# Kernel optimization log

Measured on AMD Instinct MI355X. Metric: run time of the kernel, lower is better.

## Reference

```python
import jax, jax.numpy as jnp
import numpy as np

B, S, D, H, DFF = 2, 2048, 768, 12, 3072
DK = D // H
EPS = 1e-6


def setup_inputs() -> dict:
    key = jax.random.key(0)
    ks = jax.random.split(key, 12)
    n = lambda k, shp: jax.random.normal(k, shp, jnp.float32) * 0.02
    return {
        "x": jax.random.normal(ks[0], (B, S, D), jnp.float32),
        "mask": jax.random.randint(ks[1], (1, 1, S, S), 0, 2).astype(jnp.int32),
        "wq": n(ks[2], (D, D)), "bq": jnp.zeros((D,), jnp.float32),
        "wk": n(ks[3], (D, D)), "bk": jnp.zeros((D,), jnp.float32),
        "wv": n(ks[4], (D, D)), "bv": jnp.zeros((D,), jnp.float32),
        "wo": n(ks[5], (D, D)), "bo": jnp.zeros((D,), jnp.float32),
        "w1": n(ks[6], (D, DFF)), "b1": jnp.zeros((DFF,), jnp.float32),
        "w2": n(ks[7], (DFF, D)), "b2": jnp.zeros((D,), jnp.float32),
        "alpha1": jnp.ones((D,), jnp.float32), "beta1": jnp.zeros((D,), jnp.float32),
        "alpha2": jnp.ones((D,), jnp.float32), "beta2": jnp.zeros((D,), jnp.float32),
    }


def _layernorm(x, alpha, bias):
    # Faithful to source: unbiased std (ddof=1) and eps added to std, not var.
    mean = x.mean(axis=-1, keepdims=True)
    var = jnp.sum((x - mean) ** 2, axis=-1, keepdims=True) / (x.shape[-1] - 1)
    return alpha * (x - mean) / (jnp.sqrt(var) + EPS) + bias


def reference(x, mask, wq, bq, wk, bk, wv, bv, wo, bo, w1, b1, w2, b2,
              alpha1, beta1, alpha2, beta2):
    # --- residual 1: pre-norm self-attention ---
    h = _layernorm(x, alpha1, beta1)
    q = (h @ wq + bq).reshape(B, S, H, DK).transpose(0, 2, 1, 3)  # [B,H,S,DK]
    k = (h @ wk + bk).reshape(B, S, H, DK).transpose(0, 2, 1, 3)
    v = (h @ wv + bv).reshape(B, S, H, DK).transpose(0, 2, 1, 3)
    scores = jnp.einsum('bhsd,bhtd->bhst', q, k) / jnp.sqrt(jnp.float32(DK))
    scores = jnp.where(mask == 0, jnp.float32(-1e9), scores)
    attn = jax.nn.softmax(scores, axis=-1)
    o = jnp.einsum('bhst,bhtd->bhsd', attn, v)
    o = o.transpose(0, 2, 1, 3).reshape(B, S, D)
    x = x + (o @ wo + bo)
    # --- residual 2: pre-norm FFN ---
    h2 = _layernorm(x, alpha2, beta2)
    ff = jnp.maximum(h2 @ w1 + b1, 0.0) @ w2 + b2
    return x + ff
```

## Files before the change

### kernel.cpp

```cpp
#include <hip/hip_runtime.h>

typedef unsigned short u16;
typedef unsigned int u32;
typedef unsigned long long u64;
typedef __attribute__((ext_vector_type(8))) short bf16x8;
typedef __attribute__((ext_vector_type(4))) float f32x4;
typedef __attribute__((ext_vector_type(2))) unsigned int u32x2;

#define SEQ 2048
#define DM  768
#define NH  12
#define NB  2
#define LDQ (3 * DM)

#define SCALE_Q 0.180336879f
#define NEGB   -1.44269504e9f

__device__ __forceinline__ float bf2f(u16 u) {
  union { u32 i; float f; } v; v.i = ((u32)u) << 16; return v.f;
}
__device__ __forceinline__ u16 f2bf(float f) {
  union { float f; u32 i; } v; v.f = f;
  u32 r = v.i + 0x7FFFu + ((v.i >> 16) & 1u);
  return (u16)(r >> 16);
}
__device__ __forceinline__ void gl_lds16(const u16* g, u16* l) {
  __builtin_amdgcn_global_load_lds(
      (const __attribute__((address_space(1))) unsigned int*)g,
      (__attribute__((address_space(3))) unsigned int*)l, 16, 0, 0);
}

__global__ __launch_bounds__(256) void prep_kernel(
    const float* __restrict__ wq, const float* __restrict__ wk,
    const float* __restrict__ wv, const float* __restrict__ wo,
    const float* __restrict__ w1, const float* __restrict__ w2,
    const float* __restrict__ bq, const float* __restrict__ bk,
    const float* __restrict__ bv, const int* __restrict__ mask,
    u16* __restrict__ wqkvt, u16* __restrict__ wot,
    u16* __restrict__ w1t, u16* __restrict__ w2t,
    float* __restrict__ bqkv, u64* __restrict__ mbitsT) {
  __shared__ float t[32][33];
  const int j = blockIdx.x, tid = threadIdx.x;
  const float* in = nullptr; u16* out = nullptr;
  int R = 0, C = 0, bx = 0, by = 0; float sc = 1.0f;
  if (j < 2304) {
    int which = j / 576, local = j % 576;
    in = which == 0 ? wq : which == 1 ? wk : which == 2 ? wv : wo;
    out = which == 3 ? wot : wqkvt + (size_t)which * DM * DM;
    sc = (which == 0) ? SCALE_Q : 1.0f;
    R = DM; C = DM; bx = local % 24; by = local / 24;
  } else if (j < 4608) {
    int local = j - 2304;
    in = w1; out = w1t; R = DM; C = 3072; bx = local % 96; by = local / 96;
  } else if (j < 6912) {
    int local = j - 4608;
    in = w2; out = w2t; R = 3072; C = DM; bx = local % 24; by = local / 24;
  } else if (j < 6921) {
    int i = (j - 6912) * 256 + tid;
    float v = (i < DM) ? bq[i] * SCALE_Q : (i < 2 * DM ? bk[i - DM] : bv[i - 2 * DM]);
    bqkv[i] = v;
    return;
  } else {
    int wid = (j - 6921) * 4 + (tid >> 6);
    int lane = tid & 63;
    int row = wid >> 5, word = wid & 31;
    int m = mask[(long)row * SEQ + word * 64 + lane];
    u64 bb = __ballot(m != 0);
    if (lane == 0) mbitsT[(long)word * SEQ + row] = bb;
    return;
  }
  long r0 = (long)by * 32, c0 = (long)bx * 32;
  int lc = tid & 31, wr = tid >> 5;
#pragma unroll
  for (int i = 0; i < 4; i++) {
    int row = wr + i * 8;
    t[row][lc] = in[(r0 + row) * C + c0 + lc];
  }
  __syncthreads();
#pragma unroll
  for (int i = 0; i < 4; i++) {
    int row = wr + i * 8;
    out[(c0 + row) * R + r0 + lc] = f2bf(t[lc][row] * sc);
  }
}

__global__ __launch_bounds__(256) void transpose_kernel(
    const u16* __restrict__ in, u16* __restrict__ out, int ldin, int R, int C) {
  __shared__ u16 t[32][33];
  long r0 = (long)blockIdx.y * 32, c0 = (long)blockIdx.x * 32;
  int lc = threadIdx.x & 31, wr = threadIdx.x >> 5;
#pragma unroll
  for (int i = 0; i < 4; i++) {
    int row = wr + i * 8;
    t[row][lc] = in[(r0 + row) * (long)ldin + c0 + lc];
  }
  __syncthreads();
#pragma unroll
  for (int i = 0; i < 4; i++) {
    int row = wr + i * 8;
    out[(c0 + row) * R + r0 + lc] = t[lc][row];
  }
}

__global__ __launch_bounds__(256) void ln_kernel(
    const float* __restrict__ x, const float* __restrict__ alpha,
    const float* __restrict__ beta, u16* __restrict__ out) {
  long row = blockIdx.x;
  const float* xr = x + row * DM;
  int tid = threadIdx.x;
  float v[3];
  float s = 0.f, sq = 0.f;
#pragma unroll
  for (int i = 0; i < 3; i++) {
    v[i] = xr[tid + i * 256];
    s += v[i]; sq += v[i] * v[i];
  }
#pragma unroll
  for (int off = 32; off >= 1; off >>= 1) {
    s += __shfl_down(s, off, 64);
    sq += __shfl_down(sq, off, 64);
  }
  __shared__ float ss[4], ssq[4];
  int wave = tid >> 6;
  if ((tid & 63) == 0) { ss[wave] = s; ssq[wave] = sq; }
  __syncthreads();
  float ts = ss[0] + ss[1] + ss[2] + ss[3];
  float tsq = ssq[0] + ssq[1] + ssq[2] + ssq[3];
  float mean = ts * (1.0f / (float)DM);
  float var = fmaxf((tsq - ts * mean) * (1.0f / (float)(DM - 1)), 0.0f);
  float inv = 1.0f / (sqrtf(var) + 1e-6f);
#pragma unroll
  for (int i = 0; i < 3; i++) {
    int c = tid + i * 256;
    out[row * DM + c] = f2bf(alpha[c] * (v[i] - mean) * inv + beta[c]);
  }
}

template<int BN>
__global__ __launch_bounds__(256, 2) void gemm_bt_kernel(
    const u16* __restrict__ A, const u16* __restrict__ Bt,
    const float* __restrict__ bias, const float* res,
    u16* Cb, float* Cf, int M, int N, int K, int relu) {
  constexpr int NJ = BN / 32;
  __shared__ __align__(16) u16 As[2][128][32];
  __shared__ __align__(16) u16 Bs[2][BN][32];
  const int tid = threadIdx.x;
  const int lane = tid & 63, wave = tid >> 6;
  const int g = lane >> 4, lr = lane & 15;
  const int wm = (wave >> 1) * 64, wn = (wave & 1) * (BN / 2);
  const long m0 = (long)blockIdx.y * 128;
  const long n0 = (long)blockIdx.x * BN;
  const int srow = tid >> 2;
  const int scol = (tid & 3) * 8;

  const u16* aSrc = A + (m0 + srow) * K + scol;
  const u16* bSrc = Bt + (n0 + srow) * K + scol;

  auto STAGE = [&](int buf, int k0) {
    gl_lds16(aSrc + k0, &As[buf][srow][scol]);
    gl_lds16(aSrc + (long)64 * K + k0, &As[buf][srow + 64][scol]);
    gl_lds16(bSrc + k0, &Bs[buf][srow][scol]);
    if (BN == 128) gl_lds16(bSrc + (long)64 * K + k0, &Bs[buf][srow + 64][scol]);
  };

  f32x4 acc[4][NJ];
#pragma unroll
  for (int i = 0; i < 4; i++)
#pragma unroll
    for (int j = 0; j < NJ; j++) acc[i][j] = (f32x4)0.0f;

  STAGE(0, 0);
  __syncthreads();
  const int nk = K / 32;
  for (int t = 0; t < nk; t++) {
    const int cur = t & 1;
    if (t + 1 < nk) STAGE(cur ^ 1, (t + 1) * 32);
    bf16x8 af[4], bfr[NJ];
#pragma unroll
    for (int i = 0; i < 4; i++) af[i] = *(const bf16x8*)&As[cur][wm + i * 16 + lr][g * 8];
#pragma unroll
    for (int j = 0; j < NJ; j++) bfr[j] = *(const bf16x8*)&Bs[cur][wn + j * 16 + lr][g * 8];
#pragma unroll
    for (int i = 0; i < 4; i++)
#pragma unroll
      for (int j = 0; j < NJ; j++)
        acc[i][j] = __builtin_amdgcn_mfma_f32_16x16x32_bf16(af[i], bfr[j], acc[i][j], 0, 0, 0);
    __syncthreads();
  }
#pragma unroll
  for (int j = 0; j < NJ; j++) {
    long col = n0 + wn + j * 16 + lr;
    float bv = bias[col];
#pragma unroll
    for (int i = 0; i < 4; i++) {
#pragma unroll
      for (int r = 0; r < 4; r++) {
        long row = m0 + wm + i * 16 + g * 4 + r;
        float v = acc[i][j][r] + bv;
        if (res) v += res[row * N + col];
        if (relu) v = fmaxf(v, 0.0f);
        if (Cb) Cb[row * N + col] = f2bf(v);
        else    Cf[row * N + col] = v;
      }
    }
  }
}

__global__ __launch_bounds__(256, 3) void attn_kernel(
    const u16* __restrict__ qkv, const u16* __restrict__ vt,
    const u64* __restrict__ mbitsT, u16* __restrict__ o) {
  __shared__ __align__(16) u16 Ks[2][64][64];
  __shared__ __align__(16) u16 Vs[2][64][64];
  __shared__ __align__(16) u32 Ps32[4][16][32];
  const int qt = blockIdx.x, h = blockIdx.y, b = blockIdx.z;
  const int tid = threadIdx.x;
  const int lane = tid & 63, wave = tid >> 6;
  const int g = lane >> 4, lr = lane & 15;
  const int qr0 = qt * 64 + wave * 16;

  const u16* q = qkv;
  const u16* k = qkv + DM;

  const long qbase = ((long)(b * SEQ + qr0 + lr)) * LDQ + h * 64;
  bf16x8 qf0 = *(const bf16x8*)(q + qbase + g * 8);
  bf16x8 qf1 = *(const bf16x8*)(q + qbase + 32 + g * 8);

  bf16x8 onesf;
#pragma unroll
  for (int j = 0; j < 8; j++) onesf[j] = (short)0x3F80;

  f32x4 lsum = (f32x4)0.0f;
  f32x4 oacc[4];
#pragma unroll
  for (int d = 0; d < 4; d++) oacc[d] = (f32x4)0.0f;

  const int strow = tid >> 3;
  const int stcolb = (tid & 7) * 16;
  const int swzb = stcolb ^ ((strow & 7) << 4);
  const u16* ksrc = k + (long)b * SEQ * LDQ + h * 64 + (swzb >> 1);
  const u16* vsrc = vt + ((long)(h * 64 + strow)) * (NB * SEQ) + (long)b * SEQ + (swzb >> 1);
  const int sc16 = stcolb >> 1;

  auto STAGE = [&](int buf, int kt) {
    const u16* kr = ksrc + (long)(kt * 64 + strow) * LDQ;
    gl_lds16(kr, &Ks[buf][strow][sc16]);
    gl_lds16(kr + (long)32 * LDQ, &Ks[buf][strow + 32][sc16]);
    const u16* vr = vsrc + kt * 64;
    gl_lds16(vr, &Vs[buf][strow][sc16]);
    gl_lds16(vr + 32 * (NB * SEQ), &Vs[buf][strow + 32][sc16]);
  };

  const int rs = (lr & 7) << 3;
  const int c0 = (g * 8) ^ rs;
  const int c1 = (32 + g * 8) ^ rs;

  const u64* mrow = mbitsT + (qr0 + lr);
  const int pswz = (lr & 7) << 2;
  const int pb0 = (4 * g) ^ pswz;
  const int pb1 = (16 + 4 * g) ^ pswz;

  STAGE(0, 0);
  __syncthreads();
  for (int kt = 0; kt < SEQ / 64; kt++) {
    const int cur = kt & 1;
    if (kt + 1 < SEQ / 64) STAGE(cur ^ 1, kt + 1);
    u64 mb = mrow[(long)kt * SEQ];

    f32x4 sf[4];
    __builtin_amdgcn_s_setprio(1);
#pragma unroll
    for (int n = 0; n < 4; n++) {
      bf16x8 kb0 = *(const bf16x8*)&Ks[cur][n * 16 + lr][c0];
      bf16x8 kb1 = *(const bf16x8*)&Ks[cur][n * 16 + lr][c1];
      sf[n] = __builtin_amdgcn_mfma_f32_16x16x32_bf16(kb0, qf0, (f32x4)0.0f, 0, 0, 0);
      sf[n] = __builtin_amdgcn_mfma_f32_16x16x32_bf16(kb1, qf1, sf[n], 0, 0, 0);
    }
    __builtin_amdgcn_s_setprio(0);
    u64 tsh = mb >> (4 * g);
    u32 mlo = (u32)tsh, mhi = (u32)(tsh >> 32);
#pragma unroll
    for (int n = 0; n < 4; n++) {
      u32 w = (n < 2) ? mlo : mhi;
#pragma unroll
      for (int r = 0; r < 4; r++) {
        u32 bit = 1u << (16 * (n & 1) + r);
        sf[n][r] = (w & bit) ? sf[n][r] : NEGB;
      }
    }
#pragma unroll
    for (int n = 0; n < 4; n++) {
      union { float f; u32 i; } p0, p1, p2, p3;
      p0.f = exp2f(sf[n][0]); p1.f = exp2f(sf[n][1]);
      p2.f = exp2f(sf[n][2]); p3.f = exp2f(sf[n][3]);
      u32 w0 = (p1.i & 0xFFFF0000u) | (p0.i >> 16);
      u32 w1 = (p3.i & 0xFFFF0000u) | (p2.i >> 16);
      int widx = (8 * n + 2 * g) ^ pswz;
      *(u32x2*)&Ps32[wave][lr][widx] = (u32x2){w0, w1};
    }
    asm volatile("" ::: "memory");
    bf16x8 pf0 = *(const bf16x8*)&Ps32[wave][lr][pb0];
    bf16x8 pf1 = *(const bf16x8*)&Ps32[wave][lr][pb1];
    __builtin_amdgcn_s_setprio(1);
    lsum = __builtin_amdgcn_mfma_f32_16x16x32_bf16(onesf, pf0, lsum, 0, 0, 0);
    lsum = __builtin_amdgcn_mfma_f32_16x16x32_bf16(onesf, pf1, lsum, 0, 0, 0);
#pragma unroll
    for (int db = 0; db < 4; db++) {
      bf16x8 v0 = *(const bf16x8*)&Vs[cur][db * 16 + lr][c0];
      bf16x8 v1 = *(const bf16x8*)&Vs[cur][db * 16 + lr][c1];
      oacc[db] = __builtin_amdgcn_mfma_f32_16x16x32_bf16(v0, pf0, oacc[db], 0, 0, 0);
      oacc[db] = __builtin_amdgcn_mfma_f32_16x16x32_bf16(v1, pf1, oacc[db], 0, 0, 0);
    }
    __builtin_amdgcn_s_setprio(0);
    __syncthreads();
  }
  float inv = 1.0f / lsum[0];
  long row = (long)b * SEQ + qr0 + lr;
#pragma unroll
  for (int db = 0; db < 4; db++) {
    u32 lo = ((u32)f2bf(oacc[db][1] * inv) << 16) | f2bf(oacc[db][0] * inv);
    u32 hi = ((u32)f2bf(oacc[db][3] * inv) << 16) | f2bf(oacc[db][2] * inv);
    *(u32x2*)(o + row * DM + h * 64 + db * 16 + g * 4) = (u32x2){lo, hi};
  }
}

extern "C" void kernel_launch(void* const* d_in, const int* in_sizes, int n_in,
                              void* d_out, int out_size, void* d_ws, size_t ws_size,
                              hipStream_t stream) {
  const float* x      = (const float*)d_in[0];
  const int*   mask   = (const int*)d_in[1];
  const float* wq     = (const float*)d_in[2];
  const float* bq     = (const float*)d_in[3];
  const float* wk     = (const float*)d_in[4];
  const float* bk     = (const float*)d_in[5];
  const float* wv     = (const float*)d_in[6];
  const float* bv     = (const float*)d_in[7];
  const float* wo     = (const float*)d_in[8];
  const float* bo     = (const float*)d_in[9];
  const float* w1     = (const float*)d_in[10];
  const float* b1     = (const float*)d_in[11];
  const float* w2     = (const float*)d_in[12];
  const float* b2     = (const float*)d_in[13];
  const float* alpha1 = (const float*)d_in[14];
  const float* beta1  = (const float*)d_in[15];
  const float* alpha2 = (const float*)d_in[16];
  const float* beta2  = (const float*)d_in[17];
  float* outf = (float*)d_out;

  char* ws = (char*)d_ws;
  size_t off = 0;
  auto alloc = [&](size_t bytes) {
    void* p = ws + off;
    off += (bytes + 255) & ~(size_t)255;
    return p;
  };
  const size_t DD = (size_t)DM * DM * 2;
  const size_t DF = (size_t)DM * 3072 * 2;
  const size_t ROWS = (size_t)NB * SEQ;
  const size_t ACT = ROWS * DM * 2;

  u16* wqkvt = (u16*)alloc(3 * DD);
  u16* wot   = (u16*)alloc(DD);
  u16* w1t   = (u16*)alloc(DF);
  u16* w2t   = (u16*)alloc(DF);
  float* bqkv = (float*)alloc(3 * DM * 4);
  u64* mbitsT = (u64*)alloc((size_t)(SEQ / 64) * SEQ * 8);
  u16* h     = (u16*)alloc(ACT);
  u16* qkv   = (u16*)alloc(ROWS * 3 * DM * 2);
  u16* vtb   = (u16*)alloc(ACT);
  u16* ob    = (u16*)alloc(ACT);
  u16* fb = qkv;
  u16* h2 = h;
  float* x1 = outf;

  dim3 blk(256);
  prep_kernel<<<dim3(23305), blk, 0, stream>>>(wq, wk, wv, wo, w1, w2, bq, bk, bv,
                                               mask, wqkvt, wot, w1t, w2t, bqkv, mbitsT);

  ln_kernel<<<ROWS, blk, 0, stream>>>(x, alpha1, beta1, h);
  gemm_bt_kernel<128><<<dim3(18, 32), blk, 0, stream>>>(h, wqkvt, bqkv, nullptr, qkv, nullptr, 4096, 3 * DM, 768, 0);
  transpose_kernel<<<dim3(24, 128), blk, 0, stream>>>(qkv + 2 * DM, vtb, LDQ, 4096, 768);
  attn_kernel<<<dim3(SEQ / 64, NH, NB), blk, 0, stream>>>(qkv, vtb, mbitsT, ob);
  gemm_bt_kernel<64><<<dim3(12, 32), blk, 0, stream>>>(ob, wot, bo, x, nullptr, x1, 4096, 768, 768, 0);
  ln_kernel<<<ROWS, blk, 0, stream>>>(x1, alpha2, beta2, h2);
  gemm_bt_kernel<128><<<dim3(24, 32), blk, 0, stream>>>(h2, w1t, b1, nullptr, fb, nullptr, 4096, 3072, 768, 1);
  gemm_bt_kernel<64><<<dim3(12, 32), blk, 0, stream>>>(fb, w2t, b2, x1, nullptr, outf, 4096, 768, 3072, 0);
}
```

Before: 238.3 us.

## Triple-buffer GEMM loads with vmcnt waits and remap blocks across XCDs

The GEMM kernel moves from double to triple buffering in LDS. It waits on outstanding vector-memory counts with explicit s_waitcnt and uses one barrier per k-step instead of two syncthreads, so loads for tile t+2 overlap compute on tile t. GEMM and attention launches become 1D grids with a block-index swizzle that places neighbouring tiles on the same XCD, aiming for better L2 reuse. The cost is more LDS per block and hand-tuned wait counts, which must match the number of loads each STAGE issues.

Result: faster. 220.7 us (-7.4%).

```diff
diff --git a/kernel.cpp b/kernel.cpp
--- a/kernel.cpp
+++ b/kernel.cpp
@@ -28,6 +28,11 @@
   __builtin_amdgcn_global_load_lds(
       (const __attribute__((address_space(1))) unsigned int*)g,
       (__attribute__((address_space(3))) unsigned int*)l, 16, 0, 0);
+}
+template<int N> __device__ __forceinline__ void wait_vmcnt() {
+  if constexpr (N == 0) asm volatile("s_waitcnt vmcnt(0)" ::: "memory");
+  else if constexpr (N == 3) asm volatile("s_waitcnt vmcnt(3)" ::: "memory");
+  else if constexpr (N == 4) asm volatile("s_waitcnt vmcnt(4)" ::: "memory");
 }
 
 __global__ __launch_bounds__(256) void prep_kernel(
@@ -140,23 +145,28 @@
 __global__ __launch_bounds__(256, 2) void gemm_bt_kernel(
     const u16* __restrict__ A, const u16* __restrict__ Bt,
     const float* __restrict__ bias, const float* res,
-    u16* Cb, float* Cf, int M, int N, int K, int relu) {
+    u16* Cb, float* Cf, int M, int N, int K, int relu, int nx) {
   constexpr int NJ = BN / 32;
-  __shared__ __align__(16) u16 As[2][128][32];
-  __shared__ __align__(16) u16 Bs[2][BN][32];
+  constexpr int L = (BN == 128) ? 4 : 3;
+  __shared__ __align__(16) u16 As[3][128][32];
+  __shared__ __align__(16) u16 Bs[3][BN][32];
   const int tid = threadIdx.x;
   const int lane = tid & 63, wave = tid >> 6;
   const int g = lane >> 4, lr = lane & 15;
   const int wm = (wave >> 1) * 64, wn = (wave & 1) * (BN / 2);
-  const long m0 = (long)blockIdx.y * 128;
-  const long n0 = (long)blockIdx.x * BN;
+  const int o = blockIdx.x;
+  const int wg = (o & 7) * ((int)gridDim.x >> 3) + (o >> 3);
+  const int bx = wg % nx, by = wg / nx;
+  const long m0 = (long)by * 128;
+  const long n0 = (long)bx * BN;
   const int srow = tid >> 2;
   const int scol = (tid & 3) * 8;
 
   const u16* aSrc = A + (m0 + srow) * K + scol;
   const u16* bSrc = Bt + (n0 + srow) * K + scol;
 
-  auto STAGE = [&](int buf, int k0) {
+  auto STAGE = [&](int buf, int t) {
+    const int k0 = t * 32;
     gl_lds16(aSrc + k0, &As[buf][srow][scol]);
     gl_lds16(aSrc + (long)64 * K + k0, &As[buf][srow + 64][scol]);
     gl_lds16(bSrc + k0, &Bs[buf][srow][scol]);
@@ -169,12 +179,14 @@
 #pragma unroll
     for (int j = 0; j < NJ; j++) acc[i][j] = (f32x4)0.0f;
 
+  const int nk = K / 32;
   STAGE(0, 0);
-  __syncthreads();
-  const int nk = K / 32;
+  STAGE(1, 1);
   for (int t = 0; t < nk; t++) {
-    const int cur = t & 1;
-    if (t + 1 < nk) STAGE(cur ^ 1, (t + 1) * 32);
+    const int cur = t % 3;
+    if (t + 1 < nk) wait_vmcnt<L>(); else wait_vmcnt<0>();
+    __builtin_amdgcn_sched_barrier(0);
+    __builtin_amdgcn_s_barrier();
     bf16x8 af[4], bfr[NJ];
 #pragma unroll
     for (int i = 0; i < 4; i++) af[i] = *(const bf16x8*)&As[cur][wm + i * 16 + lr][g * 8];
@@ -185,7 +197,7 @@
 #pragma unroll
       for (int j = 0; j < NJ; j++)
         acc[i][j] = __builtin_amdgcn_mfma_f32_16x16x32_bf16(af[i], bfr[j], acc[i][j], 0, 0, 0);
-    __syncthreads();
+    if (t + 2 < nk) STAGE((t + 2) % 3, t + 2);
   }
 #pragma unroll
   for (int j = 0; j < NJ; j++) {
@@ -208,11 +220,13 @@
 
 __global__ __launch_bounds__(256, 3) void attn_kernel(
     const u16* __restrict__ qkv, const u16* __restrict__ vt,
-    const u64* __restrict__ mbitsT, u16* __restrict__ o) {
+    const u64* __restrict__ mbitsT, u16* __restrict__ o_) {
   __shared__ __align__(16) u16 Ks[2][64][64];
   __shared__ __align__(16) u16 Vs[2][64][64];
   __shared__ __align__(16) u32 Ps32[4][16][32];
-  const int qt = blockIdx.x, h = blockIdx.y, b = blockIdx.z;
+  const int o = blockIdx.x;
+  const int wg = (o & 7) * 96 + (o >> 3);
+  const int qt = wg & 31, h = (wg >> 5) % NH, b = wg / (32 * NH);
   const int tid = threadIdx.x;
   const int lane = tid & 63, wave = tid >> 6;
   const int g = lane >> 4, lr = lane & 15;
@@ -319,7 +333,7 @@
   for (int db = 0; db < 4; db++) {
     u32 lo = ((u32)f2bf(oacc[db][1] * inv) << 16) | f2bf(oacc[db][0] * inv);
     u32 hi = ((u32)f2bf(oacc[db][3] * inv) << 16) | f2bf(oacc[db][2] * inv);
-    *(u32x2*)(o + row * DM + h * 64 + db * 16 + g * 4) = (u32x2){lo, hi};
+    *(u32x2*)(o_ + row * DM + h * 64 + db * 16 + g * 4) = (u32x2){lo, hi};
   }
 }
 
@@ -377,11 +391,11 @@
                                                mask, wqkvt, wot, w1t, w2t, bqkv, mbitsT);
 
   ln_kernel<<<ROWS, blk, 0, stream>>>(x, alpha1, beta1, h);
-  gemm_bt_kernel<128><<<dim3(18, 32), blk, 0, stream>>>(h, wqkvt, bqkv, nullptr, qkv, nullptr, 4096, 3 * DM, 768, 0);
+  gemm_bt_kernel<128><<<dim3(576), blk, 0, stream>>>(h, wqkvt, bqkv, nullptr, qkv, nullptr, 4096, 3 * DM, 768, 0, 18);
   transpose_kernel<<<dim3(24, 128), blk, 0, stream>>>(qkv + 2 * DM, vtb, LDQ, 4096, 768);
-  attn_kernel<<<dim3(SEQ / 64, NH, NB), blk, 0, stream>>>(qkv, vtb, mbitsT, ob);
-  gemm_bt_kernel<64><<<dim3(12, 32), blk, 0, stream>>>(ob, wot, bo, x, nullptr, x1, 4096, 768, 768, 0);
+  attn_kernel<<<dim3(32 * NH * NB), blk, 0, stream>>>(qkv, vtb, mbitsT, ob);
+  gemm_bt_kernel<64><<<dim3(384), blk, 0, stream>>>(ob, wot, bo, x, nullptr, x1, 4096, 768, 768, 0, 12);
   ln_kernel<<<ROWS, blk, 0, stream>>>(x1, alpha2, beta2, h2);
-  gemm_bt_kernel<128><<<dim3(24, 32), blk, 0, stream>>>(h2, w1t, b1, nullptr, fb, nullptr, 4096, 3072, 768, 1);
-  gemm_bt_kernel<64><<<dim3(12, 32), blk, 0, stream>>>(fb, w2t, b2, x1, nullptr, outf, 4096, 768, 3072, 0);
-}
+  gemm_bt_kernel<128><<<dim3(768), blk, 0, stream>>>(h2, w1t, b1, nullptr, fb, nullptr, 4096, 3072, 768, 1, 24);
+  gemm_bt_kernel<64><<<dim3(384), blk, 0, stream>>>(fb, w2t, b2, x1, nullptr, outf, 4096, 768, 3072, 0, 12);
+}
```
